# Performance work log

Hardware: AMD Instinct MI355X
Metric: run time of the kernel (lower is better)

## Reference

```python
import jax, jax.numpy as jnp
import numpy as np
import math

B, T, D, H = 2, 2048, 1024, 16
DK = D // H
NEG = -1e9  # finite stand-in for -inf causal fill inside the ALiBi bias


def make_alibi_bias(n_heads: int, seq_len: int) -> jnp.ndarray:
    # standard ALiBi slopes: 2^(-8*h/H) for h = 1..H
    slopes = 2.0 ** (-8.0 * (np.arange(1, n_heads + 1) / n_heads))  # [H]
    pos = np.arange(seq_len)
    dist = pos[None, :] - pos[:, None]  # [T,T], j - i
    bias = slopes[:, None, None] * dist[None, :, :]  # [H,T,T], <=0 below diag
    bias = np.where(dist[None] > 0, NEG, bias)  # causal: mask future
    return jnp.asarray(bias, dtype=jnp.float32)


def setup_inputs() -> dict:
    key = jax.random.key(0)
    ks = jax.random.split(key, 8)
    s = 0.02
    return {
        "query": jax.random.normal(ks[0], (B, T, D), jnp.float32),
        "key": jax.random.normal(ks[1], (B, T, D), jnp.float32),
        "value": jax.random.normal(ks[2], (B, T, D), jnp.float32),
        "alibi_bias": make_alibi_bias(H, T),
        "wq": jax.random.normal(ks[3], (D, D), jnp.float32) * s,
        "wk": jax.random.normal(ks[4], (D, D), jnp.float32) * s,
        "wv": jax.random.normal(ks[5], (D, D), jnp.float32) * s,
        "wo": jax.random.normal(ks[6], (D, D), jnp.float32) * s,
        "bo": jnp.zeros((D,), jnp.float32),
    }


def reference(query, key, value, alibi_bias, wq, wk, wv, wo, bo):
    b, tq, d = query.shape
    # linear projections (torch Linear: x @ W^T), split heads -> [B,H,T,d_k]
    def split(x, w):
        y = jnp.einsum('btd,ed->bte', x, w)
        return y.reshape(b, -1, H, DK).transpose(0, 2, 1, 3)
    Q, K, V = split(query, wq), split(key, wk), split(value, wv)
    # scores + ALiBi bias (bias already encodes causality)
    scores = jnp.einsum('bhqd,bhkd->bhqk', Q, K) / math.sqrt(DK)
    scores = scores + alibi_bias[None]  # broadcast over batch
    attn = jax.nn.softmax(scores, axis=-1)
    out = jnp.einsum('bhqk,bhkd->bhqd', attn, V)  # [B,H,Tq,d_k]
    out = out.transpose(0, 2, 1, 3).reshape(b, tq, d)
    return jnp.einsum('btd,ed->bte', out, wo) + bo
```

## Files before the change

kernel.cpp:

```cpp
#include <hip/hip_runtime.h>
#include <hip/hip_bf16.h>
#include <stdint.h>

#define Bc   2
#define Tc   2048
#define Dc   1024
#define Hc   16
#define DKc  64
#define BTc  4096
#define LOG2E 1.44269504088896f

typedef unsigned short u16;
typedef unsigned int u32;
typedef __attribute__((ext_vector_type(8))) short bf16x8;
typedef __attribute__((ext_vector_type(4))) float f32x4;
typedef __attribute__((ext_vector_type(2))) u32 u32x2;

static __device__ __forceinline__ u16 f2bf(float f) {
  union { float f; unsigned u; } v; v.f = f;
  unsigned r = v.u + 0x7fffu + ((v.u >> 16) & 1u);
  return (u16)(r >> 16);
}

static __device__ __forceinline__ u32 cvt_pk_bf16(float lo, float hi) {
  u32 r;
  asm volatile("v_cvt_pk_bf16_f32 %0, %1, %2" : "=v"(r) : "v"(lo), "v"(hi));
  return r;
}

static __device__ __forceinline__ f32x4 mfma16(bf16x8 a, bf16x8 b, f32x4 c) {
  return __builtin_amdgcn_mfma_f32_16x16x32_bf16(a, b, c, 0, 0, 0);
}

__global__ void conv_kernel(const float* __restrict__ q, const float* __restrict__ k,
                            const float* __restrict__ v, const float* __restrict__ wq,
                            const float* __restrict__ wk, const float* __restrict__ wv,
                            const float* __restrict__ wo,
                            u16* __restrict__ Xq, u16* __restrict__ Xk, u16* __restrict__ Xv,
                            u16* __restrict__ Wq, u16* __restrict__ Wk, u16* __restrict__ Wv,
                            u16* __restrict__ Wo) {
  int z = blockIdx.z, bx = blockIdx.x;
  const float* src; u16* dst; int i;
  if (z < 3) {
    src = z == 0 ? q : z == 1 ? k : v;
    dst = z == 0 ? Xq : z == 1 ? Xk : Xv;
    i = bx * 256 + threadIdx.x;
  } else {
    int w = bx >> 10;
    src = w == 0 ? wq : w == 1 ? wk : w == 2 ? wv : wo;
    dst = w == 0 ? Wq : w == 1 ? Wk : w == 2 ? Wv : Wo;
    i = (bx & 1023) * 256 + threadIdx.x;
  }
  float4 f = ((const float4*)src)[i];
  ushort4 r; r.x = f2bf(f.x); r.y = f2bf(f.y); r.z = f2bf(f.z); r.w = f2bf(f.w);
  ((ushort4*)dst)[i] = r;
}

#define AS1 const __attribute__((address_space(1))) void*
#define AS3 __attribute__((address_space(3))) void*

__global__ __launch_bounds__(256) void gemm_proj(const u16* __restrict__ Xq, const u16* __restrict__ Xk,
                                                 const u16* __restrict__ Xv, const u16* __restrict__ Wq,
                                                 const u16* __restrict__ Wk, const u16* __restrict__ Wv,
                                                 u16* __restrict__ Qh, u16* __restrict__ Kh,
                                                 u16* __restrict__ VTo) {
  __shared__ u16 As[2][128 * 32];
  __shared__ u16 Bs[2][128 * 32];
  int dd = blockIdx.x;
  int logical = (dd & 7) * 96 + (dd >> 3);
  int mp = logical / 24, rest = logical % 24;
  int z = rest >> 3, ny = rest & 7;
  const u16* A = z == 0 ? Xq : z == 1 ? Xk : Xv;
  const u16* W = z == 0 ? Wq : z == 1 ? Wk : Wv;
  u16* outp    = z == 0 ? Qh : z == 1 ? Kh : VTo;
  float scale = (z == 0) ? 0.125f * LOG2E : 1.0f;
  int tid = threadIdx.x;
  int lane = tid & 63, wave = tid >> 6;
  int ln = lane & 15, g = lane >> 4;
  int m0 = mp * 128, n0 = ny * 128;
  int wm = (wave >> 1) * 64, wn = (wave & 1) * 64;
  f32x4 acc[4][4] = {};
  int c0 = tid, c1 = tid + 256;
  const u16* gA0 = A + (size_t)(m0 + (c0 >> 2)) * 1024 + (c0 & 3) * 8;
  const u16* gA1 = A + (size_t)(m0 + (c1 >> 2)) * 1024 + (c1 & 3) * 8;
  const u16* gW0 = W + (size_t)(n0 + (c0 >> 2)) * 1024 + (c0 & 3) * 8;
  const u16* gW1 = W + (size_t)(n0 + (c1 >> 2)) * 1024 + (c1 & 3) * 8;

#define PSTAGE(bufi, k0_) do {                                                                 \
    __builtin_amdgcn_global_load_lds((AS1)(gA0 + (k0_)), (AS3)(&As[bufi][c0 * 8]), 16, 0, 0);  \
    __builtin_amdgcn_global_load_lds((AS1)(gA1 + (k0_)), (AS3)(&As[bufi][c1 * 8]), 16, 0, 0);  \
    __builtin_amdgcn_global_load_lds((AS1)(gW0 + (k0_)), (AS3)(&Bs[bufi][c0 * 8]), 16, 0, 0);  \
    __builtin_amdgcn_global_load_lds((AS1)(gW1 + (k0_)), (AS3)(&Bs[bufi][c1 * 8]), 16, 0, 0);  \
  } while (0)

  PSTAGE(0, 0);
  __syncthreads();
  int cur = 0;
  for (int it = 0; it < 32; ++it) {
    if (it < 31) PSTAGE(cur ^ 1, (it + 1) * 32);
    bf16x8 af[4], bfr[4];
#pragma unroll
    for (int mi = 0; mi < 4; ++mi) af[mi]  = *(const bf16x8*)&As[cur][(wm + mi * 16 + ln) * 32 + g * 8];
#pragma unroll
    for (int ni = 0; ni < 4; ++ni) bfr[ni] = *(const bf16x8*)&Bs[cur][(wn + ni * 16 + ln) * 32 + g * 8];
#pragma unroll
    for (int mi = 0; mi < 4; ++mi)
#pragma unroll
      for (int ni = 0; ni < 4; ++ni)
        acc[mi][ni] = mfma16(af[mi], bfr[ni], acc[mi][ni]);
    __syncthreads();
    cur ^= 1;
  }
#undef PSTAGE

  if (z == 2) {
#pragma unroll
    for (int mi = 0; mi < 4; ++mi)
#pragma unroll
      for (int ni = 0; ni < 4; ++ni) {
        int t0 = m0 + wm + mi * 16 + g * 4;
        int gn = n0 + wn + ni * 16 + ln;
        size_t bhead = ((size_t)(t0 >> 11)) * Hc + (gn >> 6);
        ushort4 pk;
        pk.x = f2bf(acc[mi][ni][0]); pk.y = f2bf(acc[mi][ni][1]);
        pk.z = f2bf(acc[mi][ni][2]); pk.w = f2bf(acc[mi][ni][3]);
        *(ushort4*)&outp[(bhead * DKc + (gn & 63)) * Tc + (t0 & 2047)] = pk;
      }
  } else {
#pragma unroll
    for (int mi = 0; mi < 4; ++mi)
#pragma unroll
      for (int ni = 0; ni < 4; ++ni)
#pragma unroll
        for (int r = 0; r < 4; ++r) {
          int gm = m0 + wm + mi * 16 + g * 4 + r;
          int gn = n0 + wn + ni * 16 + ln;
          size_t bhead = ((size_t)(gm >> 11)) * Hc + (gn >> 6);
          outp[(bhead * Tc + (gm & 2047)) * DKc + (gn & 63)] = f2bf(acc[mi][ni][r] * scale);
        }
  }
}

__global__ __launch_bounds__(256) void gemm_out(const u16* __restrict__ Ain, const u16* __restrict__ W,
                                                float* __restrict__ of, const float* __restrict__ bias) {
  __shared__ u16 As[2][64 * 32];
  __shared__ u16 Bs[2][128 * 32];
  int dd = blockIdx.x;
  int logical = (dd & 7) * 64 + (dd >> 3);
  int mp = logical >> 3, ny = logical & 7;
  int tid = threadIdx.x;
  int lane = tid & 63, wave = tid >> 6;
  int ln = lane & 15, g = lane >> 4;
  int m0 = mp * 64, n0 = ny * 128;
  int wm = (wave >> 1) * 32, wn = (wave & 1) * 64;
  f32x4 acc[2][4] = {};
  int ca = tid, cb0 = tid, cb1 = tid + 256;
  const u16* gA  = Ain + (size_t)(m0 + (ca  >> 2)) * 1024 + (ca  & 3) * 8;
  const u16* gW0 = W   + (size_t)(n0 + (cb0 >> 2)) * 1024 + (cb0 & 3) * 8;
  const u16* gW1 = W   + (size_t)(n0 + (cb1 >> 2)) * 1024 + (cb1 & 3) * 8;

#define OSTAGE(bufi, k0_) do {                                                                 \
    __builtin_amdgcn_global_load_lds((AS1)(gA  + (k0_)), (AS3)(&As[bufi][ca  * 8]), 16, 0, 0); \
    __builtin_amdgcn_global_load_lds((AS1)(gW0 + (k0_)), (AS3)(&Bs[bufi][cb0 * 8]), 16, 0, 0); \
    __builtin_amdgcn_global_load_lds((AS1)(gW1 + (k0_)), (AS3)(&Bs[bufi][cb1 * 8]), 16, 0, 0); \
  } while (0)

  OSTAGE(0, 0);
  __syncthreads();
  int cur = 0;
  for (int it = 0; it < 32; ++it) {
    if (it < 31) OSTAGE(cur ^ 1, (it + 1) * 32);
    bf16x8 af[2], bfr[4];
#pragma unroll
    for (int mi = 0; mi < 2; ++mi) af[mi]  = *(const bf16x8*)&As[cur][(wm + mi * 16 + ln) * 32 + g * 8];
#pragma unroll
    for (int ni = 0; ni < 4; ++ni) bfr[ni] = *(const bf16x8*)&Bs[cur][(wn + ni * 16 + ln) * 32 + g * 8];
#pragma unroll
    for (int mi = 0; mi < 2; ++mi)
#pragma unroll
      for (int ni = 0; ni < 4; ++ni)
        acc[mi][ni] = mfma16(af[mi], bfr[ni], acc[mi][ni]);
    __syncthreads();
    cur ^= 1;
  }
#undef OSTAGE

#pragma unroll
  for (int mi = 0; mi < 2; ++mi)
#pragma unroll
    for (int ni = 0; ni < 4; ++ni)
#pragma unroll
      for (int r = 0; r < 4; ++r) {
        int gm = m0 + wm + mi * 16 + g * 4 + r;
        int gn = n0 + wn + ni * 16 + ln;
        of[(size_t)gm * 1024 + gn] = acc[mi][ni][r] + bias[gn];
      }
}

__global__ __launch_bounds__(256, 2) void flash_attn(const u16* __restrict__ Qh,
                                                     const u16* __restrict__ Kh,
                                                     const u16* __restrict__ VT,
                                                     u16* __restrict__ O) {
  __shared__ u16 Ks[2][64 * 64];
  __shared__ u16 Vs[2][64 * 64];
  __shared__ u16 P_lds[8][16][64];
  int d = blockIdx.x;
  int logical = (d & 7) * 64 + (d >> 3);
  int bh = logical >> 4, pid = logical & 15;
  int qhi = 16 + pid, qlo = 15 - pid;
  int b = bh >> 4, h = bh & (Hc - 1);
  int tid = threadIdx.x, wave = tid >> 6, lane = tid & 63;
  int ln = lane & 15, g = lane >> 4;
  float slope2 = exp2f(-0.5f * (float)(h + 1)) * LOG2E;

  const u16* gK = Kh + (size_t)bh * Tc * DKc;
  const u16* gV = VT + (size_t)bh * DKc * Tc;
  int c0 = tid, c1 = tid + 256;
  int r0 = c0 >> 3, r1 = c1 >> 3;
  int e0 = ((c0 & 7) << 3) ^ ((r0 & 7) << 3);
  int e1 = ((c1 & 7) << 3) ^ ((r1 & 7) << 3);
  size_t kO0 = (size_t)r0 * DKc + e0, kO1 = (size_t)r1 * DKc + e1;
  size_t vO0 = (size_t)r0 * Tc + e0, vO1 = (size_t)r1 * Tc + e1;

#define STAGE(bufi, ks_) do {                                                                  \
    __builtin_amdgcn_global_load_lds((AS1)(gK + (size_t)(ks_) * DKc + kO0),                    \
                                     (AS3)(&Ks[bufi][c0 * 8]), 16, 0, 0);                      \
    __builtin_amdgcn_global_load_lds((AS1)(gK + (size_t)(ks_) * DKc + kO1),                    \
                                     (AS3)(&Ks[bufi][c1 * 8]), 16, 0, 0);                      \
    __builtin_amdgcn_global_load_lds((AS1)(gV + (size_t)(ks_) + vO0),                          \
                                     (AS3)(&Vs[bufi][c0 * 8]), 16, 0, 0);                      \
    __builtin_amdgcn_global_load_lds((AS1)(gV + (size_t)(ks_) + vO1),                          \
                                     (AS3)(&Vs[bufi][c1 * 8]), 16, 0, 0);                      \
  } while (0)

  int qlocal = wave * 16 + ln;
  int qgH = qhi * 64 + qlocal, qgL = qlo * 64 + qlocal;
  const u16* QpH = Qh + ((size_t)bh * Tc + qgH) * DKc;
  const u16* QpL = Qh + ((size_t)bh * Tc + qgL) * DKc;
  bf16x8 qfH0 = *(const bf16x8*)&QpH[g * 8];
  bf16x8 qfH1 = *(const bf16x8*)&QpH[32 + g * 8];
  bf16x8 qfL0 = *(const bf16x8*)&QpL[g * 8];
  bf16x8 qfL1 = *(const bf16x8*)&QpL[32 + g * 8];

  float vb[4][4];
#pragma unroll
  for (int j = 0; j < 4; ++j)
#pragma unroll
    for (int r = 0; r < 4; ++r)
      vb[j][r] = slope2 * (float)(j * 16 + g * 4 + r);

  f32x4 accH[4] = {}, accL[4] = {};
  float MH = -1e30f, LH = 0.f, ML = -1e30f, LL = 0.f;

  auto tile_step = [&](int buf, int ks, bool diag, bf16x8 qf0, bf16x8 qf1,
                       int qg, float& Mx, float& Lx, f32x4* accO, int pslot) {
    f32x4 s[4] = {};
    __builtin_amdgcn_s_setprio(1);
#pragma unroll
    for (int j = 0; j < 4; ++j) {
      int row = j * 16 + ln, sw = (row & 7) << 3;
      bf16x8 kf0 = *(const bf16x8*)&Ks[buf][row * DKc + ((g * 8) ^ sw)];
      bf16x8 kf1 = *(const bf16x8*)&Ks[buf][row * DKc + ((32 + g * 8) ^ sw)];
      s[j] = mfma16(kf0, qf0, s[j]);
      s[j] = mfma16(kf1, qf1, s[j]);
    }
    __builtin_amdgcn_s_setprio(0);
    float vv[4][4];
    float mloc = -1e30f;
#pragma unroll
    for (int j = 0; j < 4; ++j)
#pragma unroll
      for (int r = 0; r < 4; ++r) {
        float t = s[j][r] + vb[j][r];
        if (diag) t = (j * 16 + g * 4 + r > qlocal) ? -1e30f : t;
        vv[j][r] = t;
        mloc = fmaxf(mloc, t);
      }
    mloc = fmaxf(mloc, __shfl_xor(mloc, 16, 64));
    mloc = fmaxf(mloc, __shfl_xor(mloc, 32, 64));
    float cterm = slope2 * (float)(ks - qg);
    float mc = mloc + cterm;
    if (__any(mc > Mx)) {
      float newM = fmaxf(Mx, mc);
      float sc = __builtin_amdgcn_exp2f(Mx - newM);
      Mx = newM;
      Lx *= sc;
      float scb[4];
#pragma unroll
      for (int r = 0; r < 4; ++r) scb[r] = __shfl(sc, g * 4 + r, 64);
#pragma unroll
      for (int nd = 0; nd < 4; ++nd)
#pragma unroll
        for (int r = 0; r < 4; ++r) accO[nd][r] *= scb[r];
    }
    float dsub = Mx - cterm;
    float rs = 0.f;
#pragma unroll
    for (int j = 0; j < 4; ++j)
#pragma unroll
      for (int r = 0; r < 4; ++r) {
        float p = __builtin_amdgcn_exp2f(vv[j][r] - dsub);
        vv[j][r] = p;
        rs += p;
      }
    Lx += rs;
    char* Prow = (char*)&P_lds[pslot][ln][0];
    int psw = (ln & 7) << 4;
#pragma unroll
    for (int j = 0; j < 4; ++j) {
      u32x2 w;
      w.x = cvt_pk_bf16(vv[j][0], vv[j][1]);
      w.y = cvt_pk_bf16(vv[j][2], vv[j][3]);
      *(u32x2*)(Prow + ((j * 32 + g * 8) ^ psw)) = w;
    }
    __builtin_amdgcn_s_setprio(1);
#pragma unroll
    for (int kk = 0; kk < 2; ++kk) {
      bf16x8 pa = *(const bf16x8*)(Prow + ((kk * 64 + g * 16) ^ psw));
#pragma unroll
      for (int nd = 0; nd < 4; ++nd) {
        int d2 = nd * 16 + ln, o = kk * 32 + g * 8;
        bf16x8 vf = *(const bf16x8*)&Vs[buf][d2 * DKc + (o ^ ((d2 & 7) << 3))];
        accO[nd] = mfma16(pa, vf, accO[nd]);
      }
    }
    __builtin_amdgcn_s_setprio(0);
  };

  STAGE(0, qhi * 64);
  __syncthreads();
  int buf = 0;
  for (int kb = qhi; kb >= 0; --kb) {
    int ks = kb * 64;
    if (kb > 0) STAGE(buf ^ 1, ks - 64);
    tile_step(buf, ks, kb == qhi, qfH0, qfH1, qgH, MH, LH, accH, wave);
    if (kb <= qlo)
      tile_step(buf, ks, kb == qlo, qfL0, qfL1, qgL, ML, LL, accL, wave + 4);
    __syncthreads();
    buf ^= 1;
  }

#pragma unroll
  for (int tile = 0; tile < 2; ++tile) {
    float Lx = tile ? LL : LH;
    f32x4* accO = tile ? accL : accH;
    int qb = tile ? qlo : qhi;
    float Lf = Lx + __shfl_xor(Lx, 16, 64);
    Lf = Lf + __shfl_xor(Lf, 32, 64);
    float linv[4];
#pragma unroll
    for (int r = 0; r < 4; ++r) linv[r] = 1.0f / __shfl(Lf, g * 4 + r, 64);
#pragma unroll
    for (int nd = 0; nd < 4; ++nd)
#pragma unroll
      for (int r = 0; r < 4; ++r) {
        int t = qb * 64 + wave * 16 + g * 4 + r;
        int dcol = h * 64 + nd * 16 + ln;
        O[((size_t)(b * Tc + t)) * Dc + dcol] = f2bf(accO[nd][r] * linv[r]);
      }
  }
#undef STAGE
}

extern "C" void kernel_launch(void* const* d_in, const int* in_sizes, int n_in,
                              void* d_out, int out_size, void* d_ws, size_t ws_size,
                              hipStream_t stream) {
  const float* q  = (const float*)d_in[0];
  const float* k  = (const float*)d_in[1];
  const float* v  = (const float*)d_in[2];
  const float* wq = (const float*)d_in[4];
  const float* wk = (const float*)d_in[5];
  const float* wv = (const float*)d_in[6];
  const float* wo = (const float*)d_in[7];
  const float* bo = (const float*)d_in[8];

  char* ws = (char*)d_ws;
  const size_t MB = 1024 * 1024;
  u16* Xq = (u16*)(ws + 0 * MB);
  u16* Xk = (u16*)(ws + 8 * MB);
  u16* Xv = (u16*)(ws + 16 * MB);
  u16* Wq = (u16*)(ws + 24 * MB);
  u16* Wk = (u16*)(ws + 26 * MB);
  u16* Wv = (u16*)(ws + 28 * MB);
  u16* Wo = (u16*)(ws + 30 * MB);
  u16* Qh = (u16*)(ws + 32 * MB);
  u16* Kh = (u16*)(ws + 40 * MB);
  u16* VT = (u16*)(ws + 48 * MB);
  u16* Ob = (u16*)(ws + 56 * MB);
  float* out = (float*)d_out;

  conv_kernel<<<dim3(4096, 1, 4), 256, 0, stream>>>(q, k, v, wq, wk, wv, wo,
                                                    Xq, Xk, Xv, Wq, Wk, Wv, Wo);
  gemm_proj<<<dim3(768), 256, 0, stream>>>(Xq, Xk, Xv, Wq, Wk, Wv, Qh, Kh, VT);
  flash_attn<<<dim3(512), 256, 0, stream>>>(Qh, Kh, VT, Ob);
  gemm_out<<<dim3(512), 256, 0, stream>>>(Ob, Wo, out, bo);
}
```

Before: 116.9 us.

## Triple-buffer LDS staging with vmcnt waits and single barrier per iteration

Converts the double-buffered global-to-LDS pipelines in both GEMMs and the flash-attention kernel into three-stage ring buffers, prefetching two tiles ahead. Each iteration waits on vmcnt for the oldest stage, then issues one barrier, replacing the full __syncthreads before and after compute. This is meant to hide global load latency and halve barrier count. The cost is more LDS per block, which may lower occupancy in flash_attn, and correctness now relies on exact vmcnt counts per stage.

```diff
diff --git a/kernel.cpp b/kernel.cpp
--- a/kernel.cpp
+++ b/kernel.cpp
@@ -31,6 +31,8 @@
 static __device__ __forceinline__ f32x4 mfma16(bf16x8 a, bf16x8 b, f32x4 c) {
   return __builtin_amdgcn_mfma_f32_16x16x32_bf16(a, b, c, 0, 0, 0);
 }
+
+#define VMCNT(n) asm volatile("s_waitcnt vmcnt(" #n ")" ::: "memory")
 
 __global__ void conv_kernel(const float* __restrict__ q, const float* __restrict__ k,
                             const float* __restrict__ v, const float* __restrict__ wq,
@@ -64,8 +66,8 @@
                                                  const u16* __restrict__ Wk, const u16* __restrict__ Wv,
                                                  u16* __restrict__ Qh, u16* __restrict__ Kh,
                                                  u16* __restrict__ VTo) {
-  __shared__ u16 As[2][128 * 32];
-  __shared__ u16 Bs[2][128 * 32];
+  __shared__ u16 As[3][128 * 32];
+  __shared__ u16 Bs[3][128 * 32];
   int dd = blockIdx.x;
   int logical = (dd & 7) * 96 + (dd >> 3);
   int mp = logical / 24, rest = logical % 24;
@@ -94,10 +96,12 @@
   } while (0)
 
   PSTAGE(0, 0);
-  __syncthreads();
-  int cur = 0;
+  PSTAGE(1, 32);
   for (int it = 0; it < 32; ++it) {
-    if (it < 31) PSTAGE(cur ^ 1, (it + 1) * 32);
+    if (it < 31) VMCNT(4); else VMCNT(0);
+    __builtin_amdgcn_s_barrier();
+    if (it < 30) PSTAGE((it + 2) % 3, (it + 2) * 32);
+    int cur = it % 3;
     bf16x8 af[4], bfr[4];
 #pragma unroll
     for (int mi = 0; mi < 4; ++mi) af[mi]  = *(const bf16x8*)&As[cur][(wm + mi * 16 + ln) * 32 + g * 8];
@@ -108,8 +112,6 @@
 #pragma unroll
       for (int ni = 0; ni < 4; ++ni)
         acc[mi][ni] = mfma16(af[mi], bfr[ni], acc[mi][ni]);
-    __syncthreads();
-    cur ^= 1;
   }
 #undef PSTAGE
 
@@ -143,8 +145,8 @@
 
 __global__ __launch_bounds__(256) void gemm_out(const u16* __restrict__ Ain, const u16* __restrict__ W,
                                                 float* __restrict__ of, const float* __restrict__ bias) {
-  __shared__ u16 As[2][64 * 32];
-  __shared__ u16 Bs[2][128 * 32];
+  __shared__ u16 As[3][64 * 32];
+  __shared__ u16 Bs[3][128 * 32];
   int dd = blockIdx.x;
   int logical = (dd & 7) * 64 + (dd >> 3);
   int mp = logical >> 3, ny = logical & 7;
@@ -166,10 +168,12 @@
   } while (0)
 
   OSTAGE(0, 0);
-  __syncthreads();
-  int cur = 0;
+  OSTAGE(1, 32);
   for (int it = 0; it < 32; ++it) {
-    if (it < 31) OSTAGE(cur ^ 1, (it + 1) * 32);
+    if (it < 31) VMCNT(3); else VMCNT(0);
+    __builtin_amdgcn_s_barrier();
+    if (it < 30) OSTAGE((it + 2) % 3, (it + 2) * 32);
+    int cur = it % 3;
     bf16x8 af[2], bfr[4];
 #pragma unroll
     for (int mi = 0; mi < 2; ++mi) af[mi]  = *(const bf16x8*)&As[cur][(wm + mi * 16 + ln) * 32 + g * 8];
@@ -180,8 +184,6 @@
 #pragma unroll
       for (int ni = 0; ni < 4; ++ni)
         acc[mi][ni] = mfma16(af[mi], bfr[ni], acc[mi][ni]);
-    __syncthreads();
-    cur ^= 1;
   }
 #undef OSTAGE
 
@@ -201,8 +203,8 @@
                                                      const u16* __restrict__ Kh,
                                                      const u16* __restrict__ VT,
                                                      u16* __restrict__ O) {
-  __shared__ u16 Ks[2][64 * 64];
-  __shared__ u16 Vs[2][64 * 64];
+  __shared__ u16 Ks[3][64 * 64];
+  __shared__ u16 Vs[3][64 * 64];
   __shared__ u16 P_lds[8][16][64];
   int d = blockIdx.x;
   int logical = (d & 7) * 64 + (d >> 3);
@@ -328,16 +330,17 @@
   };
 
   STAGE(0, qhi * 64);
-  __syncthreads();
-  int buf = 0;
-  for (int kb = qhi; kb >= 0; --kb) {
+  STAGE(1, (qhi - 1) * 64);
+  for (int t = 0; t <= qhi; ++t) {
+    int kb = qhi - t;
+    if (kb > 0) VMCNT(4); else VMCNT(0);
+    __builtin_amdgcn_s_barrier();
+    if (kb >= 2) STAGE((t + 2) % 3, (kb - 2) * 64);
+    int buf = t % 3;
     int ks = kb * 64;
-    if (kb > 0) STAGE(buf ^ 1, ks - 64);
     tile_step(buf, ks, kb == qhi, qfH0, qfH1, qgH, MH, LH, accH, wave);
     if (kb <= qlo)
       tile_step(buf, ks, kb == qlo, qfL0, qfL1, qgL, ML, LL, accL, wave + 4);
-    __syncthreads();
-    buf ^= 1;
   }
 
 #pragma unroll
```

New measurement: 120.2 us. 2.8% more time.
